# Optimization experiments

Hardware: AMD Instinct MI355X
Metric: run time of the kernel (lower is better)

## Reference

```python
import jax, jax.numpy as jnp
import numpy as np

B, T, E = 64, 512, 512          # batch, seq_len, embedding_size
H2 = 512                        # per-direction hidden = hidden_size // 2
V = 32000                       # vocab
PAD = 0                         # padding_idx


def _lstm_scan(x_tbe, mask_tb, Wih, Whh, bih, bhh):
    """Masked LSTMCell loop over time (PyTorch gate order i,f,g,o).
    x_tbe: (T,B,E) time-major, mask_tb: (T,B). Returns (out (T,B,H), hT, cT)."""
    Bn = x_tbe.shape[1]
    Hn = Whh.shape[1]
    h0 = jnp.zeros((Bn, Hn), x_tbe.dtype)
    c0 = jnp.zeros((Bn, Hn), x_tbe.dtype)

    def step(carry, xm):
        h, c = carry
        x, m = xm
        gates = x @ Wih.T + bih + h @ Whh.T + bhh  # (B, 4H)
        i, f, g, o = jnp.split(gates, 4, axis=-1)
        i = jax.nn.sigmoid(i)
        f = jax.nn.sigmoid(f)
        o = jax.nn.sigmoid(o)
        g = jnp.tanh(g)
        c_new = f * c + i * g
        h_new = o * jnp.tanh(c_new)
        m = m[:, None]
        # masked update: padded steps carry state through unchanged
        h_new = h_new * m + h * (1.0 - m)
        c_new = c_new * m + c * (1.0 - m)
        return (h_new, c_new), h_new

    (hT, cT), out = jax.lax.scan(step, (h0, c0), (x_tbe, mask_tb))
    return out, hT, cT


def _encoder(inputs, lengths, emb_table, Wih_f, Whh_f, bih_f, bhh_f,
             Wih_b, Whh_b, bih_b, bhh_b):
    table = emb_table.at[PAD].set(0.0)      # padding_idx row is zero
    embeds = table[inputs]                  # (B,T,E); dropout p=0 -> no-op
    mask = (jnp.arange(T)[None, :] < lengths[:, None]).astype(embeds.dtype)  # (B,T)
    x = embeds.transpose(1, 0, 2)           # (T,B,E) time-major
    m = mask.T                              # (T,B)
    out_f, ht_f, ct_f = _lstm_scan(x, m, Wih_f, Whh_f, bih_f, bhh_f)
    out_b, ht_b, ct_b = _lstm_scan(x[::-1], m[::-1], Wih_b, Whh_b, bih_b, bhh_b)
    output = jnp.concatenate([out_f, out_b[::-1]], axis=2)   # (T,B,2*H2)
    ht = jnp.concatenate([ht_f, ht_b], axis=1)               # (B,2*H2) (squeezed num_layers=1)
    ct = jnp.concatenate([ct_f, ct_b], axis=1)
    return output.transpose(1, 0, 2), ht, ct, mask           # output (B,T,H)


def setup_inputs() -> dict:
    key = jax.random.key(0)
    ks = jax.random.split(key, 12)
    s_e = 1.0 / np.sqrt(E)
    s_h = 1.0 / np.sqrt(H2)
    inp = {
        "inputs": jax.random.randint(ks[0], (B, T), 0, V, dtype=jnp.int64 if jax.config.jax_enable_x64 else jnp.int32),
        "lengths": jax.random.randint(ks[1], (B,), 1, T + 1, dtype=jnp.int64 if jax.config.jax_enable_x64 else jnp.int32),
        "emb_table": jax.random.normal(ks[2], (V, E), jnp.float32) * 0.02,
        "Wih_f": jax.random.normal(ks[3], (4 * H2, E), jnp.float32) * s_e,
        "Whh_f": jax.random.normal(ks[4], (4 * H2, H2), jnp.float32) * s_h,
        "bih_f": jax.random.normal(ks[5], (4 * H2,), jnp.float32) * s_h,
        "bhh_f": jax.random.normal(ks[6], (4 * H2,), jnp.float32) * s_h,
        "Wih_b": jax.random.normal(ks[7], (4 * H2, E), jnp.float32) * s_e,
        "Whh_b": jax.random.normal(ks[8], (4 * H2, H2), jnp.float32) * s_h,
        "bih_b": jax.random.normal(ks[9], (4 * H2,), jnp.float32) * s_h,
        "bhh_b": jax.random.normal(ks[10], (4 * H2,), jnp.float32) * s_h,
    }
    return inp


def reference(inputs, lengths, emb_table, Wih_f, Whh_f, bih_f, bhh_f,
              Wih_b, Whh_b, bih_b, bhh_b):
    return _encoder(inputs, lengths, emb_table, Wih_f, Whh_f, bih_f, bhh_f,
                    Wih_b, Whh_b, bih_b, bhh_b)
```

## Files before the change

### kernel.cpp

```cpp
#include <hip/hip_runtime.h>


#define Bn 64
#define Tn 512
#define NWG 64
#define TC 32
#define NCH 16

#define OUT_HT  33554432u
#define OUT_CT  33619968u
#define OUT_MSK 33685504u

#define WS_WCAT 0ull
#define WS_GX0  8388608ull
#define WS_GX1  25165824ull
#define WS_REC  41943040ull
#define WS_HST  42467328ull
#define WS_CST  42729472ull

typedef __bf16 v8bf __attribute__((ext_vector_type(8)));
typedef float  v4f  __attribute__((ext_vector_type(4)));
typedef unsigned v4u __attribute__((ext_vector_type(4)));
typedef unsigned v2u __attribute__((ext_vector_type(2)));

__device__ __forceinline__ unsigned short f2bf(float f) {
    unsigned u = __float_as_uint(f);
    u = (u + 0x7FFFu + ((u >> 16) & 1u)) >> 16;
    return (unsigned short)u;
}

__device__ __forceinline__ void bf2x(unsigned u, float& lo, float& hi) {
    lo = __uint_as_float(u << 16);
    hi = __uint_as_float(u & 0xffff0000u);
}

__device__ __forceinline__ v8bf ldfrag(const unsigned short* p) {
    return *reinterpret_cast<const v8bf*>(p);
}

__device__ __forceinline__ v4u ld_co16(const void* p) {
    v4u r;
    asm volatile("global_load_dwordx4 %0, %1, off sc0 sc1" : "=v"(r) : "v"(p));
    return r;
}

__device__ __forceinline__ float fsig(float x) {
    return 1.0f / (1.0f + __expf(-x));
}
__device__ __forceinline__ float ftanh(float x) {
    x = fminf(fmaxf(x, -15.0f), 15.0f);
    float e = __expf(2.0f * x);
    return (e - 1.0f) / (e + 1.0f);
}


__global__ void k_weights(const float* __restrict__ Wih_f, const float* __restrict__ Whh_f,
                          const float* __restrict__ Wih_b, const float* __restrict__ Whh_b,
                          unsigned short* __restrict__ Wcat) {
    int idx = blockIdx.x * 256 + threadIdx.x;
    if (idx >= 2 * 2048 * 256) return;
    int k4 = idx & 255;
    int n  = (idx >> 8) & 2047;
    int d  = idx >> 19;
    int k  = k4 * 4;
    const float* src;
    if (k < 512) src = (d ? Wih_b : Wih_f) + (size_t)n * 512 + k;
    else         src = (d ? Whh_b : Whh_f) + (size_t)n * 512 + (k - 512);
    float4 v = *(const float4*)src;
    unsigned short o[4] = { f2bf(v.x), f2bf(v.y), f2bf(v.z), f2bf(v.w) };
    *(ushort4*)(Wcat + (size_t)idx * 4) = *(const ushort4*)o;
}

__global__ void k_zero(unsigned char* __restrict__ recb,
                       float* __restrict__ hstate, float* __restrict__ cstate) {
    int i = blockIdx.x * 256 + threadIdx.x;
    if (i < 32768) { v4u z = {0,0,0,0}; ((v4u*)recb)[i] = z; }
    if (i < 65536) { hstate[i] = 0.0f; cstate[i] = 0.0f; }
}

__global__ void k_mask(const int* __restrict__ lengths, float* __restrict__ mask_out) {
    int i = blockIdx.x * 256 + threadIdx.x;
    if (i >= Bn * Tn) return;
    int b = i >> 9, t = i & 511;
    mask_out[i] = (t < lengths[b]) ? 1.0f : 0.0f;
}


__device__ __forceinline__ void gx_unit(
    unsigned short* __restrict__ Bs,
    const int* __restrict__ inputs,
    const float* __restrict__ table,
    const unsigned short* __restrict__ Wcat,
    const float* __restrict__ bih, const float* __restrict__ bhh,
    unsigned short* __restrict__ gxw,
    int d, int slg, int nt, int s0,
    int tid)
{
    const int lane = tid & 63, wave = tid >> 6;
    const int l15  = lane & 15, kq = lane >> 4;
    const int n0   = nt * 128;

    const unsigned short* Wd = Wcat + (size_t)d * (2048 * 1024);

    #pragma unroll
    for (int i = 0; i < 32; ++i) {
        int w = i * 256 + tid;
        int r = w >> 6, c = w & 63;
        v4u tmp = *(const v4u*)(Wd + (size_t)(n0 + r) * 1024 + c * 8);
        *(v4u*)&Bs[r * 512 + ((c ^ (r & 7)) * 8)] = tmp;
    }

    float bv[8];
    #pragma unroll
    for (int n2 = 0; n2 < 8; ++n2) {
        int n = n0 + n2 * 16 + l15;
        bv[n2] = bih[n] + bhh[n];
    }
    __syncthreads();

    const int ab   = wave * 16 + l15;
    const int brow = wave * 16 + kq * 4;

    #pragma unroll 1
    for (int q = 0; q < 4; ++q) {
        const int sl = slg * 4 + q;
        const int s  = s0 + sl;
        const int t  = d ? (511 - s) : s;
        const int tok = inputs[ab * 512 + t];

        v8bf af[16];
        if (tok != 0) {
            const float* tr = table + (size_t)tok * 512 + kq * 8;
            #pragma unroll
            for (int ks = 0; ks < 16; ++ks) {
                float4 v0 = *(const float4*)(tr + ks * 32);
                float4 v1 = *(const float4*)(tr + ks * 32 + 4);
                unsigned short o[8] = { f2bf(v0.x), f2bf(v0.y), f2bf(v0.z), f2bf(v0.w),
                                        f2bf(v1.x), f2bf(v1.y), f2bf(v1.z), f2bf(v1.w) };
                af[ks] = *(const v8bf*)o;
            }
        } else {
            v4u z = {0u, 0u, 0u, 0u};
            #pragma unroll
            for (int ks = 0; ks < 16; ++ks) af[ks] = __builtin_bit_cast(v8bf, z);
        }

        unsigned short* gbase = gxw + ((size_t)(d * TC + sl) * 64) * 2048;
        #pragma unroll
        for (int n2 = 0; n2 < 8; ++n2) {
            v4f acc = {0, 0, 0, 0};
            const int rb = n2 * 16 + l15;
            const unsigned short* bbp = Bs + rb * 512;
            const int sw = rb & 7;
            #pragma unroll
            for (int ks = 0; ks < 16; ++ks) {
                v8bf bf = *(const v8bf*)&bbp[((ks * 4 + kq) ^ sw) * 8];
                acc = __builtin_amdgcn_mfma_f32_16x16x32_bf16(af[ks], bf, acc, 0, 0, 0);
            }
            const int n = n0 + n2 * 16 + l15;
            #pragma unroll
            for (int qq = 0; qq < 4; ++qq)
                gbase[(size_t)(brow + qq) * 2048 + n] = f2bf(acc[qq] + bv[n2]);
        }
    }
}


__global__ __launch_bounds__(256) void k_gx(
    const int* __restrict__ inputs,
    const float* __restrict__ table,
    const unsigned short* __restrict__ Wcat,
    const float* __restrict__ bih_f, const float* __restrict__ bhh_f,
    const float* __restrict__ bih_b, const float* __restrict__ bhh_b,
    unsigned short* __restrict__ gxw, int s0)
{
    __shared__ unsigned short Bs[128 * 512];
    const int bi  = blockIdx.x;
    const int nt  = bi >> 4;
    const int d   = (bi >> 3) & 1;
    const int slg = bi & 7;
    gx_unit(Bs, inputs, table, Wcat,
            d ? bih_b : bih_f, d ? bhh_b : bhh_f,
            gxw, d, slg, nt, s0, threadIdx.x);
}


__global__ __launch_bounds__(256, 1) void fused(
    const unsigned short* __restrict__ Wcat,
    unsigned char* __restrict__ recb,
    const unsigned short* __restrict__ gxb_rd,
    unsigned short* __restrict__ gxb_wr,
    const int* __restrict__ inputs,
    const float* __restrict__ table,
    const float* __restrict__ bih_f, const float* __restrict__ bhh_f,
    const float* __restrict__ bih_b, const float* __restrict__ bhh_b,
    const int* __restrict__ lengths,
    float* __restrict__ out,
    float* __restrict__ hstate,
    float* __restrict__ cstate,
    int s0, int next_s0)
{
    __shared__ __align__(16) unsigned char smem[131072];

    if (blockIdx.x >= 64) {
        if (next_s0 < 0) return;
        const int gxi = blockIdx.x - 64;
        const int slg = gxi & 7;
        const int np  = (gxi >> 3) & 7;
        const int d   = gxi >> 6;
        unsigned short* Bs = (unsigned short*)smem;
        const float* bih = d ? bih_b : bih_f;
        const float* bhh = d ? bhh_b : bhh_f;
        #pragma unroll 1
        for (int w2 = 0; w2 < 2; ++w2) {
            gx_unit(Bs, inputs, table, Wcat, bih, bhh,
                    gxb_wr, d, slg, np * 2 + w2, next_s0, threadIdx.x);
            __syncthreads();
        }
        return;
    }

    unsigned short* hA = (unsigned short*)smem;
    float (*gLds)[65]  = reinterpret_cast<float(*)[65]>(smem + 65536);
    float (*hS)[17]    = reinterpret_cast<float(*)[17]>(smem + 82176);
    float (*cS)[17]    = reinterpret_cast<float(*)[17]>(smem + 86528);
    int* lenS          = reinterpret_cast<int*>(smem + 90880);

    const int wg   = blockIdx.x;
    const int dir  = wg >> 5;
    const int hc0  = (wg & 31) * 16;
    const int tid  = threadIdx.x;
    const int lane = tid & 63;
    const int wave = tid >> 6;
    const int wm   = wave >> 1, wn = wave & 1;
    const int l15  = lane & 15, kq = lane >> 4;
    const int eb   = tid >> 2, ejg = tid & 3;

    {
        const size_t so = (size_t)dir * (64 * 512) + (size_t)eb * 512 + hc0 + ejg * 4;
        v4f hv = *(const v4f*)(hstate + so);
        v4f cv = *(const v4f*)(cstate + so);
        #pragma unroll
        for (int jj = 0; jj < 4; ++jj) { hS[eb][ejg * 4 + jj] = hv[jj]; cS[eb][ejg * 4 + jj] = cv[jj]; }
        if (tid < 64) lenS[tid] = lengths[tid];
    }

    const unsigned short* Wd = Wcat + (size_t)dir * (2048 * 1024);
    const int rowA0 = 32 * wm + l15, rowA1 = rowA0 + 16;
    const int n0 = (2 * wn + 0) * 512 + hc0 + l15;
    const int n1 = (2 * wn + 1) * 512 + hc0 + l15;
    const unsigned short* pB0 = Wd + (size_t)n0 * 1024 + kq * 8;
    const unsigned short* pB1 = Wd + (size_t)n1 * 1024 + kq * 8;

    v8bf whB0[16], whB1[16];
    #pragma unroll
    for (int ks = 0; ks < 16; ++ks) {
        whB0[ks] = ldfrag(pB0 + (16 + ks) * 32);
        whB1[ks] = ldfrag(pB1 + (16 + ks) * 32);
    }

    const unsigned short* lA0 = hA + rowA0 * 512;
    const unsigned short* lA1 = hA + rowA1 * 512;
    const int swA0 = (rowA0 & 7) << 3, swA1 = (rowA1 & 7) << 3;

    unsigned char* recD = recb + (size_t)dir * 262144;

    __syncthreads();

    for (int sl = 0; sl < TC; ++sl) {
        const int s = s0 + sl;
        const int t = dir ? (511 - s) : s;
        const unsigned want = (unsigned)s;

        v2u gw0, gw1, gw2, gw3;
        {
            const unsigned short* g = gxb_rd + ((size_t)(dir * TC + sl) * 64 + eb) * 2048 + hc0 + ejg * 4;
            gw0 = *(const v2u*)(g);
            gw1 = *(const v2u*)(g + 512);
            gw2 = *(const v2u*)(g + 1024);
            gw3 = *(const v2u*)(g + 1536);
        }

        unsigned char* rp = recD + (size_t)(s & 1) * 131072;
        #pragma unroll
        for (int grp = 0; grp < 4; ++grp) {
            v4u r[8];
            #pragma unroll
            for (int i = 0; i < 8; ++i)
                r[i] = ld_co16(rp + (size_t)((grp * 8 + i) * 256 + tid) * 16);
            asm volatile("s_waitcnt vmcnt(0)" ::: "memory");
            __builtin_amdgcn_sched_barrier(0);
            unsigned stale = 0u;
            #pragma unroll
            for (int i = 0; i < 8; ++i) {
                int idx = (grp * 8 + i) * 256 + tid;
                if (r[i][3] == want) {
                    int b = idx >> 7, j4 = idx & 127;
                    v2u hv = { r[i][0], r[i][1] };
                    *(v2u*)&hA[b * 512 + ((j4 * 4) ^ ((b & 7) << 3))] = hv;
                } else {
                    stale |= (1u << i);
                }
            }
            while (__any(stale != 0u)) {
                v4u q[8];
                #pragma unroll
                for (int i = 0; i < 8; ++i)
                    q[i] = ld_co16(rp + (size_t)((grp * 8 + i) * 256 + tid) * 16);
                asm volatile("s_waitcnt vmcnt(0)" ::: "memory");
                __builtin_amdgcn_sched_barrier(0);
                #pragma unroll
                for (int i = 0; i < 8; ++i) {
                    if ((stale & (1u << i)) && q[i][3] == want) {
                        int idx = (grp * 8 + i) * 256 + tid;
                        int b = idx >> 7, j4 = idx & 127;
                        v2u hv = { q[i][0], q[i][1] };
                        *(v2u*)&hA[b * 512 + ((j4 * 4) ^ ((b & 7) << 3))] = hv;
                        stale &= ~(1u << i);
                    }
                }
            }
        }
        __syncthreads();

        v4f a00 = {0,0,0,0}, a01 = {0,0,0,0}, a10 = {0,0,0,0}, a11 = {0,0,0,0};
        #pragma unroll
        for (int ks = 0; ks < 16; ++ks) {
            v8bf fa0 = *(const v8bf*)&lA0[(kq * 8 + ks * 32) ^ swA0];
            v8bf fa1 = *(const v8bf*)&lA1[(kq * 8 + ks * 32) ^ swA1];
            a00 = __builtin_amdgcn_mfma_f32_16x16x32_bf16(fa0, whB0[ks], a00, 0, 0, 0);
            a01 = __builtin_amdgcn_mfma_f32_16x16x32_bf16(fa0, whB1[ks], a01, 0, 0, 0);
            a10 = __builtin_amdgcn_mfma_f32_16x16x32_bf16(fa1, whB0[ks], a10, 0, 0, 0);
            a11 = __builtin_amdgcn_mfma_f32_16x16x32_bf16(fa1, whB1[ks], a11, 0, 0, 0);
        }

        {
            int c0 = 32 * wn + l15;
            int rr = 32 * wm + kq * 4;
            #pragma unroll
            for (int q = 0; q < 4; ++q) {
                gLds[rr + q][c0     ] = a00[q];
                gLds[rr + q][c0 + 16] = a01[q];
                gLds[rr + 16 + q][c0     ] = a10[q];
                gLds[rr + 16 + q][c0 + 16] = a11[q];
            }
        }
        __syncthreads();

        {
            const int b = eb, jg = ejg;
            const int msk = (t < lenS[b]);
            float gxi[4], gxf[4], gxg[4], gxo[4];
            bf2x(gw0[0], gxi[0], gxi[1]); bf2x(gw0[1], gxi[2], gxi[3]);
            bf2x(gw1[0], gxf[0], gxf[1]); bf2x(gw1[1], gxf[2], gxf[3]);
            bf2x(gw2[0], gxg[0], gxg[1]); bf2x(gw2[1], gxg[2], gxg[3]);
            bf2x(gw3[0], gxo[0], gxo[1]); bf2x(gw3[1], gxo[2], gxo[3]);
            float hn[4], cn[4];
            #pragma unroll
            for (int jj = 0; jj < 4; ++jj) {
                int j = jg * 4 + jj;
                float gi = gLds[b][j]      + gxi[jj];
                float gf = gLds[b][16 + j] + gxf[jj];
                float gg = gLds[b][32 + j] + gxg[jj];
                float go = gLds[b][48 + j] + gxo[jj];
                float i_ = fsig(gi), f_ = fsig(gf), o_ = fsig(go), g_ = ftanh(gg);
                float c_old = cS[b][j], h_old = hS[b][j];
                float c_new = fmaf(f_, c_old, i_ * g_);
                float h_new = o_ * ftanh(c_new);
                if (!msk) { c_new = c_old; h_new = h_old; }
                cS[b][j] = c_new;
                hS[b][j] = h_new;
                hn[jj] = h_new; cn[jj] = c_new;
            }
            if (s < 511) {
                unsigned short q0 = f2bf(hn[0]), q1 = f2bf(hn[1]), q2 = f2bf(hn[2]), q3 = f2bf(hn[3]);
                v4u pk = { (unsigned)q0 | ((unsigned)q1 << 16),
                           (unsigned)q2 | ((unsigned)q3 << 16),
                           0u, (unsigned)(s + 1) };
                int idxp = b * 128 + (wg & 31) * 4 + jg;
                unsigned char* dst = recD + (size_t)((s + 1) & 1) * 131072 + (size_t)idxp * 16;
                asm volatile("global_store_dwordx4 %0, %1, off sc0 sc1" :: "v"(dst), "v"(pk) : "memory");
            }
            v4f ov = {hn[0], hn[1], hn[2], hn[3]};
            *(v4f*)&out[((size_t)b * 512 + t) * 1024 + (size_t)dir * 512 + hc0 + jg * 4] = ov;
            if (s == 511) {
                v4f cv2 = {cn[0], cn[1], cn[2], cn[3]};
                *(v4f*)&out[OUT_HT + (size_t)b * 1024 + dir * 512 + hc0 + jg * 4] = ov;
                *(v4f*)&out[OUT_CT + (size_t)b * 1024 + dir * 512 + hc0 + jg * 4] = cv2;
            }
        }
        __syncthreads();
    }

    {
        float hv[4], cv[4];
        #pragma unroll
        for (int jj = 0; jj < 4; ++jj) { hv[jj] = hS[eb][ejg * 4 + jj]; cv[jj] = cS[eb][ejg * 4 + jj]; }
        const size_t so = (size_t)dir * (64 * 512) + (size_t)eb * 512 + hc0 + ejg * 4;
        *(v4f*)(hstate + so) = *(v4f*)hv;
        *(v4f*)(cstate + so) = *(v4f*)cv;
    }
}


extern "C" void kernel_launch(void* const* d_in, const int* in_sizes, int n_in,
                              void* d_out, int out_size, void* d_ws, size_t ws_size,
                              hipStream_t stream) {
    (void)in_sizes; (void)n_in; (void)out_size; (void)ws_size;

    const int*   inputs  = (const int*)d_in[0];
    const int*   lengths = (const int*)d_in[1];
    const float* table   = (const float*)d_in[2];
    const float* Wih_f   = (const float*)d_in[3];
    const float* Whh_f   = (const float*)d_in[4];
    const float* bih_f   = (const float*)d_in[5];
    const float* bhh_f   = (const float*)d_in[6];
    const float* Wih_b   = (const float*)d_in[7];
    const float* Whh_b   = (const float*)d_in[8];
    const float* bih_b   = (const float*)d_in[9];
    const float* bhh_b   = (const float*)d_in[10];
    float* out = (float*)d_out;

    char* w = (char*)d_ws;
    unsigned short* Wcat   = (unsigned short*)(w + WS_WCAT);
    unsigned short* gxb0   = (unsigned short*)(w + WS_GX0);
    unsigned short* gxb1   = (unsigned short*)(w + WS_GX1);
    unsigned char*  recb   = (unsigned char*)(w + WS_REC);
    float*          hstate = (float*)(w + WS_HST);
    float*          cstate = (float*)(w + WS_CST);
    unsigned short* gxb[2] = { gxb0, gxb1 };

    k_weights<<<4096, 256, 0, stream>>>(Wih_f, Whh_f, Wih_b, Whh_b, Wcat);
    k_zero<<<256, 256, 0, stream>>>(recb, hstate, cstate);
    k_mask<<<128, 256, 0, stream>>>(lengths, out + OUT_MSK);

    k_gx<<<256, 256, 0, stream>>>(inputs, table, Wcat,
                                  bih_f, bhh_f, bih_b, bhh_b, gxb0, 0);

    for (int ch = 0; ch < NCH; ++ch) {
        const int next_s0 = (ch < NCH - 1) ? (ch + 1) * TC : -1;
        fused<<<192, 256, 0, stream>>>(Wcat, recb, gxb[ch & 1], gxb[(ch + 1) & 1],
                                       inputs, table,
                                       bih_f, bhh_f, bih_b, bhh_b,
                                       lengths, out, hstate, cstate,
                                       ch * TC, next_s0);
    }
}
```

Measured before the change: 3.589 ms.

## Shrink side gx workers to 16 blocks streaming weights from global memory

The fused kernel's side workers that precompute input projections for the next chunk drop from 128 to 16 blocks. Each now computes all 2048 gate columns for two timesteps at once, reading weight fragments straight from global memory instead of staging them in LDS. Fused LDS use shrinks to what the recurrent part needs. The aim is to stop the side work from competing with the 64 latency-bound recurrent workgroups for CUs and LDS. The cost is that each gx block carries far more serial work and more global traffic, which could lengthen chunks if it no longer hides behind the recurrence.

Result: slower. 9.783 ms (+172.6%).

```diff
diff --git a/kernel.cpp b/kernel.cpp
--- a/kernel.cpp
+++ b/kernel.cpp
@@ -86,82 +86,26 @@
 }
 
 
-__device__ __forceinline__ void gx_unit(
-    unsigned short* __restrict__ Bs,
-    const int* __restrict__ inputs,
-    const float* __restrict__ table,
-    const unsigned short* __restrict__ Wcat,
-    const float* __restrict__ bih, const float* __restrict__ bhh,
-    unsigned short* __restrict__ gxw,
-    int d, int slg, int nt, int s0,
-    int tid)
+__device__ __forceinline__ void gather_af(
+    const int* __restrict__ inputs, const float* __restrict__ table,
+    int d, int s, int ab, v8bf* af, int kq)
 {
-    const int lane = tid & 63, wave = tid >> 6;
-    const int l15  = lane & 15, kq = lane >> 4;
-    const int n0   = nt * 128;
-
-    const unsigned short* Wd = Wcat + (size_t)d * (2048 * 1024);
-
-    #pragma unroll
-    for (int i = 0; i < 32; ++i) {
-        int w = i * 256 + tid;
-        int r = w >> 6, c = w & 63;
-        v4u tmp = *(const v4u*)(Wd + (size_t)(n0 + r) * 1024 + c * 8);
-        *(v4u*)&Bs[r * 512 + ((c ^ (r & 7)) * 8)] = tmp;
-    }
-
-    float bv[8];
-    #pragma unroll
-    for (int n2 = 0; n2 < 8; ++n2) {
-        int n = n0 + n2 * 16 + l15;
-        bv[n2] = bih[n] + bhh[n];
-    }
-    __syncthreads();
-
-    const int ab   = wave * 16 + l15;
-    const int brow = wave * 16 + kq * 4;
-
-    #pragma unroll 1
-    for (int q = 0; q < 4; ++q) {
-        const int sl = slg * 4 + q;
-        const int s  = s0 + sl;
-        const int t  = d ? (511 - s) : s;
-        const int tok = inputs[ab * 512 + t];
-
-        v8bf af[16];
-        if (tok != 0) {
-            const float* tr = table + (size_t)tok * 512 + kq * 8;
-            #pragma unroll
-            for (int ks = 0; ks < 16; ++ks) {
-                float4 v0 = *(const float4*)(tr + ks * 32);
-                float4 v1 = *(const float4*)(tr + ks * 32 + 4);
-                unsigned short o[8] = { f2bf(v0.x), f2bf(v0.y), f2bf(v0.z), f2bf(v0.w),
-                                        f2bf(v1.x), f2bf(v1.y), f2bf(v1.z), f2bf(v1.w) };
-                af[ks] = *(const v8bf*)o;
-            }
-        } else {
-            v4u z = {0u, 0u, 0u, 0u};
-            #pragma unroll
-            for (int ks = 0; ks < 16; ++ks) af[ks] = __builtin_bit_cast(v8bf, z);
-        }
-
-        unsigned short* gbase = gxw + ((size_t)(d * TC + sl) * 64) * 2048;
-        #pragma unroll
-        for (int n2 = 0; n2 < 8; ++n2) {
-            v4f acc = {0, 0, 0, 0};
-            const int rb = n2 * 16 + l15;
-            const unsigned short* bbp = Bs + rb * 512;
-            const int sw = rb & 7;
-            #pragma unroll
-            for (int ks = 0; ks < 16; ++ks) {
-                v8bf bf = *(const v8bf*)&bbp[((ks * 4 + kq) ^ sw) * 8];
-                acc = __builtin_amdgcn_mfma_f32_16x16x32_bf16(af[ks], bf, acc, 0, 0, 0);
-            }
-            const int n = n0 + n2 * 16 + l15;
-            #pragma unroll
-            for (int qq = 0; qq < 4; ++qq)
-                gbase[(size_t)(brow + qq) * 2048 + n] = f2bf(acc[qq] + bv[n2]);
-        }
+    const int t   = d ? (511 - s) : s;
+    const int tok = inputs[ab * 512 + t];
+    if (tok != 0) {
+        const float* tr = table + (size_t)tok * 512 + kq * 8;
+        #pragma unroll
+        for (int ks = 0; ks < 16; ++ks) {
+            float4 v0 = *(const float4*)(tr + ks * 32);
+            float4 v1 = *(const float4*)(tr + ks * 32 + 4);
+            unsigned short o[8] = { f2bf(v0.x), f2bf(v0.y), f2bf(v0.z), f2bf(v0.w),
+                                    f2bf(v1.x), f2bf(v1.y), f2bf(v1.z), f2bf(v1.w) };
+            af[ks] = *(const v8bf*)o;
+        }
+    } else {
+        v4u z = {0u, 0u, 0u, 0u};
+        #pragma unroll
+        for (int ks = 0; ks < 16; ++ks) af[ks] = __builtin_bit_cast(v8bf, z);
     }
 }
 
@@ -175,13 +119,62 @@
     unsigned short* __restrict__ gxw, int s0)
 {
     __shared__ unsigned short Bs[128 * 512];
-    const int bi  = blockIdx.x;
-    const int nt  = bi >> 4;
-    const int d   = (bi >> 3) & 1;
-    const int slg = bi & 7;
-    gx_unit(Bs, inputs, table, Wcat,
-            d ? bih_b : bih_f, d ? bhh_b : bhh_f,
-            gxw, d, slg, nt, s0, threadIdx.x);
+    const int bi   = blockIdx.x;
+    const int nt   = bi >> 4;
+    const int d    = (bi >> 3) & 1;
+    const int slg  = bi & 7;
+    const int n0   = nt * 128;
+    const int tid  = threadIdx.x;
+    const int lane = tid & 63, wave = tid >> 6;
+    const int l15  = lane & 15, kq = lane >> 4;
+
+    const unsigned short* Wd = Wcat + (size_t)d * (2048 * 1024);
+
+    #pragma unroll
+    for (int i = 0; i < 32; ++i) {
+        int w = i * 256 + tid;
+        int r = w >> 6, c = w & 63;
+        v4u tmp = *(const v4u*)(Wd + (size_t)(n0 + r) * 1024 + c * 8);
+        *(v4u*)&Bs[r * 512 + ((c ^ (r & 7)) * 8)] = tmp;
+    }
+
+    const float* bih = d ? bih_b : bih_f;
+    const float* bhh = d ? bhh_b : bhh_f;
+    float bv[8];
+    #pragma unroll
+    for (int n2 = 0; n2 < 8; ++n2) {
+        int n = n0 + n2 * 16 + l15;
+        bv[n2] = bih[n] + bhh[n];
+    }
+    __syncthreads();
+
+    const int ab   = wave * 16 + l15;
+    const int brow = wave * 16 + kq * 4;
+
+    #pragma unroll 1
+    for (int q = 0; q < 4; ++q) {
+        const int sl = slg * 4 + q;
+        v8bf af[16];
+        gather_af(inputs, table, d, s0 + sl, ab, af, kq);
+
+        unsigned short* gbase = gxw + ((size_t)(d * TC + sl) * 64) * 2048;
+        #pragma unroll
+        for (int n2 = 0; n2 < 8; ++n2) {
+            v4f acc = {0, 0, 0, 0};
+            const int rb = n2 * 16 + l15;
+            const unsigned short* bbp = Bs + rb * 512;
+            const int sw = rb & 7;
+            #pragma unroll
+            for (int ks = 0; ks < 16; ++ks) {
+                v8bf bf = *(const v8bf*)&bbp[((ks * 4 + kq) ^ sw) * 8];
+                acc = __builtin_amdgcn_mfma_f32_16x16x32_bf16(af[ks], bf, acc, 0, 0, 0);
+            }
+            const int n = n0 + n2 * 16 + l15;
+            #pragma unroll
+            for (int qq = 0; qq < 4; ++qq)
+                gbase[(size_t)(brow + qq) * 2048 + n] = f2bf(acc[qq] + bv[n2]);
+        }
+    }
 }
 
 
@@ -200,22 +193,54 @@
     float* __restrict__ cstate,
     int s0, int next_s0)
 {
-    __shared__ __align__(16) unsigned char smem[131072];
+    __shared__ __align__(16) unsigned char smem[92160];
+
+    const int tid = threadIdx.x;
 
     if (blockIdx.x >= 64) {
         if (next_s0 < 0) return;
         const int gxi = blockIdx.x - 64;
         const int slg = gxi & 7;
-        const int np  = (gxi >> 3) & 7;
-        const int d   = gxi >> 6;
-        unsigned short* Bs = (unsigned short*)smem;
+        const int d   = gxi >> 3;
+        const int lane = tid & 63, wave = tid >> 6;
+        const int l15  = lane & 15, kq = lane >> 4;
+        const int ab   = wave * 16 + l15;
+        const int brow = wave * 16 + kq * 4;
+        const unsigned short* Wd = Wcat + (size_t)d * (2048 * 1024);
         const float* bih = d ? bih_b : bih_f;
         const float* bhh = d ? bhh_b : bhh_f;
+
         #pragma unroll 1
-        for (int w2 = 0; w2 < 2; ++w2) {
-            gx_unit(Bs, inputs, table, Wcat, bih, bhh,
-                    gxb_wr, d, slg, np * 2 + w2, next_s0, threadIdx.x);
-            __syncthreads();
+        for (int sp = 0; sp < 2; ++sp) {
+            const int sl0 = slg * 4 + sp * 2;
+            v8bf af0[16], af1[16];
+            gather_af(inputs, table, d, next_s0 + sl0,     ab, af0, kq);
+            gather_af(inputs, table, d, next_s0 + sl0 + 1, ab, af1, kq);
+
+            unsigned short* g0 = gxb_wr + ((size_t)(d * TC + sl0    ) * 64) * 2048;
+            unsigned short* g1 = gxb_wr + ((size_t)(d * TC + sl0 + 1) * 64) * 2048;
+
+            #pragma unroll 1
+            for (int nt = 0; nt < 16; ++nt) {
+                #pragma unroll 1
+                for (int n2 = 0; n2 < 8; ++n2) {
+                    const int n = nt * 128 + n2 * 16 + l15;
+                    const unsigned short* bp = Wd + (size_t)n * 1024 + kq * 8;
+                    v4f acc0 = {0, 0, 0, 0}, acc1 = {0, 0, 0, 0};
+                    #pragma unroll
+                    for (int ks = 0; ks < 16; ++ks) {
+                        v8bf bf = ldfrag(bp + ks * 32);
+                        acc0 = __builtin_amdgcn_mfma_f32_16x16x32_bf16(af0[ks], bf, acc0, 0, 0, 0);
+                        acc1 = __builtin_amdgcn_mfma_f32_16x16x32_bf16(af1[ks], bf, acc1, 0, 0, 0);
+                    }
+                    const float bv = bih[n] + bhh[n];
+                    #pragma unroll
+                    for (int qq = 0; qq < 4; ++qq) {
+                        g0[(size_t)(brow + qq) * 2048 + n] = f2bf(acc0[qq] + bv);
+                        g1[(size_t)(brow + qq) * 2048 + n] = f2bf(acc1[qq] + bv);
+                    }
+                }
+            }
         }
         return;
     }
@@ -229,7 +254,6 @@
     const int wg   = blockIdx.x;
     const int dir  = wg >> 5;
     const int hc0  = (wg & 31) * 16;
-    const int tid  = threadIdx.x;
     const int lane = tid & 63;
     const int wave = tid >> 6;
     const int wm   = wave >> 1, wn = wave & 1;
@@ -439,10 +463,10 @@
 
     for (int ch = 0; ch < NCH; ++ch) {
         const int next_s0 = (ch < NCH - 1) ? (ch + 1) * TC : -1;
-        fused<<<192, 256, 0, stream>>>(Wcat, recb, gxb[ch & 1], gxb[(ch + 1) & 1],
-                                       inputs, table,
-                                       bih_f, bhh_f, bih_b, bhh_b,
-                                       lengths, out, hstate, cstate,
-                                       ch * TC, next_s0);
-    }
-}
+        fused<<<80, 256, 0, stream>>>(Wcat, recb, gxb[ch & 1], gxb[(ch + 1) & 1],
+                                      inputs, table,
+                                      bih_f, bhh_f, bih_b, bhh_b,
+                                      lengths, out, hstate, cstate,
+                                      ch * TC, next_s0);
+    }
+}
```
